# Kernel optimization log

Measured on AMD Instinct MI355X. Metric: run time of the kernel, lower is better.

## Reference

```python
import jax, jax.numpy as jnp
import numpy as np

NUM_CLASSES = 10

def setup_inputs() -> dict:
    key = jax.random.key(0)
    k1, k2, k3 = jax.random.split(key, 3)
    B, D, M = 65536, 512, 16
    x = jax.random.normal(k1, (B, D), dtype=jnp.float32)
    W = jax.random.normal(k2, (M, D, NUM_CLASSES), dtype=jnp.float32) * 0.02
    b = jax.random.normal(k3, (M, NUM_CLASSES), dtype=jnp.float32) * 0.02
    return {"x": x, "W": W, "b": b}

def reference(x, W, b):
    # Each committee member is a linear classifier: logits[m] = x @ W[m] + b[m]
    logits = jnp.einsum('bd,mdc->mbc', x, W) + b[:, None, :]   # [M, B, C]
    votes = jnp.argmax(logits, axis=-1)                        # [M, B] int
    # Per-sample histogram of votes over models (torch bincount(minlength=10)),
    # vectorized as a one-hot sum over the model axis -> [B, C] float.
    hist = jnp.sum(jax.nn.one_hot(votes, NUM_CLASSES, dtype=jnp.float32), axis=0)
    return hist
```

## Files before the change

### kernel.cpp

```cpp
#include <hip/hip_runtime.h>


#define NB_ROWS 64
#define DDIM    512
#define NCLS    10
#define KCHUNK  64
#define NCHUNK  (DDIM / KCHUNK)

__global__ __launch_bounds__(1024, 2)
void committee_kernel(const float* __restrict__ x,
                      const float* __restrict__ W,
                      const float* __restrict__ bias,
                      float* __restrict__ out)
{
    __shared__ float4 xs[2][16][65];
    __shared__ int ihist[NB_ROWS * NCLS];

    const int tid  = threadIdx.x;
    const int row0 = blockIdx.x * NB_ROWS;

    if (tid < NB_ROWS * NCLS) ihist[tid] = 0;

    const int m    = __builtin_amdgcn_readfirstlane(tid >> 6);
    const int lane = tid & 63;

    const float* wp = W + (size_t)m * DDIM * NCLS;

    float acc[NCLS];
#pragma unroll
    for (int c = 0; c < NCLS; ++c) acc[c] = bias[m * NCLS + c];

    const int srow = tid >> 4;
    const int skq  = tid & 15;
    const float* gsrc = x + (size_t)(row0 + srow) * DDIM + (skq << 2);

    float4 pa = *reinterpret_cast<const float4*>(gsrc);
    xs[0][skq][srow] = pa;
    pa = *reinterpret_cast<const float4*>(gsrc + KCHUNK);

    for (int ch = 0; ch < NCHUNK; ++ch) {
        __syncthreads();
        const int cur = ch & 1;

        if (ch + 1 < NCHUNK) {
            xs[cur ^ 1][skq][srow] = pa;
            if (ch + 2 < NCHUNK) {
                pa = *reinterpret_cast<const float4*>(
                    gsrc + (size_t)(ch + 2) * KCHUNK);
            }
        }

#pragma unroll
        for (int kq = 0; kq < 16; ++kq) {
            const float4 xv = xs[cur][kq][lane];
            const float xarr[4] = {xv.x, xv.y, xv.z, xv.w};
            const float* wk = wp + (size_t)(ch * KCHUNK + (kq << 2)) * NCLS;
#pragma unroll
            for (int j = 0; j < 4; ++j) {
                const float xj = xarr[j];
#pragma unroll
                for (int c = 0; c < NCLS; ++c)
                    acc[c] = fmaf(xj, wk[j * NCLS + c], acc[c]);
            }
        }
    }

    int best = 0;
    float bv = acc[0];
#pragma unroll
    for (int c = 1; c < NCLS; ++c) {
        if (acc[c] > bv) { bv = acc[c]; best = c; }
    }

    atomicAdd(&ihist[lane * NCLS + best], 1);
    __syncthreads();

    if (tid < NB_ROWS * NCLS) {
        out[(size_t)row0 * NCLS + tid] = (float)ihist[tid];
    }
}

extern "C" void kernel_launch(void* const* d_in, const int* in_sizes, int n_in,
                              void* d_out, int out_size, void* d_ws, size_t ws_size,
                              hipStream_t stream) {
    const float* x  = (const float*)d_in[0];
    const float* W  = (const float*)d_in[1];
    const float* b  = (const float*)d_in[2];
    float* out      = (float*)d_out;

    const int nblocks = 65536 / NB_ROWS;
    committee_kernel<<<nblocks, 1024, 0, stream>>>(x, W, b, out);
}
```

Measured before the change: 166.9 us.

## Split models across block groups with 256-row tiles and atomic histogram merge

```diff
diff --git a/kernel.cpp b/kernel.cpp
--- a/kernel.cpp
+++ b/kernel.cpp
@@ -1,28 +1,37 @@
 #include <hip/hip_runtime.h>
 
 
-#define NB_ROWS 64
 #define DDIM    512
 #define NCLS    10
-#define KCHUNK  64
+#define ROWS    256
+#define KCHUNK  32
 #define NCHUNK  (DDIM / KCHUNK)
+#define ROWP    257
 
-__global__ __launch_bounds__(1024, 2)
+__global__ void zero_out_kernel(float* __restrict__ out, int n)
+{
+    const int i = blockIdx.x * 1024 + threadIdx.x;
+    if (i < n) out[i] = 0.0f;
+}
+
+__global__ __launch_bounds__(1024)
 void committee_kernel(const float* __restrict__ x,
                       const float* __restrict__ W,
                       const float* __restrict__ bias,
                       float* __restrict__ out)
 {
-    __shared__ float4 xs[2][16][65];
-    __shared__ int ihist[NB_ROWS * NCLS];
+    __shared__ float4 xs[2][8][ROWP];
+    __shared__ int ihist[ROWS * NCLS];
 
-    const int tid  = threadIdx.x;
-    const int row0 = blockIdx.x * NB_ROWS;
+    const int tid      = threadIdx.x;
+    const int rowchunk = blockIdx.x & 255;
+    const int group    = blockIdx.x >> 8;
+    const int row0     = rowchunk << 8;
 
-    if (tid < NB_ROWS * NCLS) ihist[tid] = 0;
+    for (int i = tid; i < ROWS * NCLS; i += 1024) ihist[i] = 0;
 
-    const int m    = __builtin_amdgcn_readfirstlane(tid >> 6);
-    const int lane = tid & 63;
+    const int m = (group << 2) + __builtin_amdgcn_readfirstlane(tid >> 8);
+    const int rowbase = tid & 255;
 
     const float* wp = W + (size_t)m * DDIM * NCLS;
 
@@ -30,29 +39,36 @@
 #pragma unroll
     for (int c = 0; c < NCLS; ++c) acc[c] = bias[m * NCLS + c];
 
-    const int srow = tid >> 4;
-    const int skq  = tid & 15;
-    const float* gsrc = x + (size_t)(row0 + srow) * DDIM + (skq << 2);
+    const int srow = tid >> 3;
+    const int skq  = tid & 7;
+    const float* gsrc0 = x + (size_t)(row0 + srow) * DDIM + (skq << 2);
+    const float* gsrc1 = gsrc0 + (size_t)128 * DDIM;
 
-    float4 pa = *reinterpret_cast<const float4*>(gsrc);
-    xs[0][skq][srow] = pa;
-    pa = *reinterpret_cast<const float4*>(gsrc + KCHUNK);
+    float4 pa0 = *reinterpret_cast<const float4*>(gsrc0);
+    float4 pa1 = *reinterpret_cast<const float4*>(gsrc1);
+    xs[0][skq][srow]       = pa0;
+    xs[0][skq][128 + srow] = pa1;
+    pa0 = *reinterpret_cast<const float4*>(gsrc0 + KCHUNK);
+    pa1 = *reinterpret_cast<const float4*>(gsrc1 + KCHUNK);
 
     for (int ch = 0; ch < NCHUNK; ++ch) {
         __syncthreads();
         const int cur = ch & 1;
 
         if (ch + 1 < NCHUNK) {
-            xs[cur ^ 1][skq][srow] = pa;
+            xs[cur ^ 1][skq][srow]       = pa0;
+            xs[cur ^ 1][skq][128 + srow] = pa1;
             if (ch + 2 < NCHUNK) {
-                pa = *reinterpret_cast<const float4*>(
-                    gsrc + (size_t)(ch + 2) * KCHUNK);
+                pa0 = *reinterpret_cast<const float4*>(
+                    gsrc0 + (size_t)(ch + 2) * KCHUNK);
+                pa1 = *reinterpret_cast<const float4*>(
+                    gsrc1 + (size_t)(ch + 2) * KCHUNK);
             }
         }
 
 #pragma unroll
-        for (int kq = 0; kq < 16; ++kq) {
-            const float4 xv = xs[cur][kq][lane];
+        for (int kq = 0; kq < 8; ++kq) {
+            const float4 xv = xs[cur][kq][rowbase];
             const float xarr[4] = {xv.x, xv.y, xv.z, xv.w};
             const float* wk = wp + (size_t)(ch * KCHUNK + (kq << 2)) * NCLS;
 #pragma unroll
@@ -71,12 +87,11 @@
     for (int c = 1; c < NCLS; ++c) {
         if (acc[c] > bv) { bv = acc[c]; best = c; }
     }
-
-    atomicAdd(&ihist[lane * NCLS + best], 1);
+    atomicAdd(&ihist[rowbase * NCLS + best], 1);
     __syncthreads();
 
-    if (tid < NB_ROWS * NCLS) {
-        out[(size_t)row0 * NCLS + tid] = (float)ihist[tid];
+    for (int i = tid; i < ROWS * NCLS; i += 1024) {
+        atomicAdd(&out[(size_t)row0 * NCLS + i], (float)ihist[i]);
     }
 }
 
@@ -88,6 +103,7 @@
     const float* b  = (const float*)d_in[2];
     float* out      = (float*)d_out;
 
-    const int nblocks = 65536 / NB_ROWS;
-    committee_kernel<<<nblocks, 1024, 0, stream>>>(x, W, b, out);
+    zero_out_kernel<<<(out_size + 1023) / 1024, 1024, 0, stream>>>(out, out_size);
+
+    committee_kernel<<<1024, 1024, 0, stream>>>(x, W, b, out);
 }
```

Measured after the change: 201.3 us. +20.6%, slower.

## Stage W chunks in LDS with double buffering and halve the K chunk

Applied to the files above, without the earlier changes.

```diff
diff --git a/kernel.cpp b/kernel.cpp
--- a/kernel.cpp
+++ b/kernel.cpp
@@ -4,16 +4,19 @@
 #define NB_ROWS 64
 #define DDIM    512
 #define NCLS    10
-#define KCHUNK  64
+#define KCHUNK  32
 #define NCHUNK  (DDIM / KCHUNK)
+#define WCH4    80
+#define WTOT4   (16 * WCH4)
 
-__global__ __launch_bounds__(1024, 2)
+__global__ __launch_bounds__(1024, 8)
 void committee_kernel(const float* __restrict__ x,
                       const float* __restrict__ W,
                       const float* __restrict__ bias,
                       float* __restrict__ out)
 {
-    __shared__ float4 xs[2][16][65];
+    __shared__ float4 xs[2][8][65];
+    __shared__ float4 ws4[2][WTOT4];
     __shared__ int ihist[NB_ROWS * NCLS];
 
     const int tid  = threadIdx.x;
@@ -24,43 +27,61 @@
     const int m    = __builtin_amdgcn_readfirstlane(tid >> 6);
     const int lane = tid & 63;
 
-    const float* wp = W + (size_t)m * DDIM * NCLS;
-
     float acc[NCLS];
 #pragma unroll
     for (int c = 0; c < NCLS; ++c) acc[c] = bias[m * NCLS + c];
 
-    const int srow = tid >> 4;
-    const int skq  = tid & 15;
+    const int srow = tid >> 3;
+    const int skq  = tid & 7;
     const float* gsrc = x + (size_t)(row0 + srow) * DDIM + (skq << 2);
+    const float4* W4 = reinterpret_cast<const float4*>(W);
+    const int i4a = tid;
+    const int i4b = tid + 1024;
+    const int ma  = i4a / WCH4, oa = i4a % WCH4;
+    const int mb  = i4b / WCH4, ob = i4b % WCH4;
+    #define WGIDX(mm, ch, off) ((size_t)(mm) * 1280 + (size_t)(ch) * WCH4 + (off))
 
-    float4 pa = *reinterpret_cast<const float4*>(gsrc);
-    xs[0][skq][srow] = pa;
-    pa = *reinterpret_cast<const float4*>(gsrc + KCHUNK);
+    if (tid < 512) xs[0][skq][srow] = *reinterpret_cast<const float4*>(gsrc);
+    ws4[0][i4a] = W4[WGIDX(ma, 0, oa)];
+    if (tid < 256) ws4[0][i4b] = W4[WGIDX(mb, 0, ob)];
+
+    float4 px, pw0, pw1;
+    if (tid < 512) px = *reinterpret_cast<const float4*>(gsrc + KCHUNK);
+    pw0 = W4[WGIDX(ma, 1, oa)];
+    if (tid < 256) pw1 = W4[WGIDX(mb, 1, ob)];
 
     for (int ch = 0; ch < NCHUNK; ++ch) {
         __syncthreads();
         const int cur = ch & 1;
 
         if (ch + 1 < NCHUNK) {
-            xs[cur ^ 1][skq][srow] = pa;
+            if (tid < 512) xs[cur ^ 1][skq][srow] = px;
+            ws4[cur ^ 1][i4a] = pw0;
+            if (tid < 256) ws4[cur ^ 1][i4b] = pw1;
             if (ch + 2 < NCHUNK) {
-                pa = *reinterpret_cast<const float4*>(
-                    gsrc + (size_t)(ch + 2) * KCHUNK);
+                if (tid < 512)
+                    px = *reinterpret_cast<const float4*>(
+                        gsrc + (size_t)(ch + 2) * KCHUNK);
+                pw0 = W4[WGIDX(ma, ch + 2, oa)];
+                if (tid < 256) pw1 = W4[WGIDX(mb, ch + 2, ob)];
             }
         }
 
 #pragma unroll
-        for (int kq = 0; kq < 16; ++kq) {
+        for (int kq = 0; kq < 8; ++kq) {
             const float4 xv = xs[cur][kq][lane];
             const float xarr[4] = {xv.x, xv.y, xv.z, xv.w};
-            const float* wk = wp + (size_t)(ch * KCHUNK + (kq << 2)) * NCLS;
 #pragma unroll
-            for (int j = 0; j < 4; ++j) {
-                const float xj = xarr[j];
+            for (int q = 0; q < 10; ++q) {
+                const float4 wv = ws4[cur][m * WCH4 + kq * 10 + q];
+                const float warr[4] = {wv.x, wv.y, wv.z, wv.w};
 #pragma unroll
-                for (int c = 0; c < NCLS; ++c)
-                    acc[c] = fmaf(xj, wk[j * NCLS + c], acc[c]);
+                for (int k = 0; k < 4; ++k) {
+                    const int f = 4 * q + k;
+                    const int j = f / 10;
+                    const int c = f % 10;
+                    acc[c] = fmaf(xarr[j], warr[k], acc[c]);
+                }
             }
         }
     }
```

Measured after the change: 210.3 us. 26.0% more time.
